# Optimization experiments

Measured on AMD Instinct MI355X. Metric: run time of the kernel, lower is better.

The kernel has to match this reference:

```python
import jax, jax.numpy as jnp
import numpy as np

N_LEVELS = 16
F_PER_LEVEL = 2
LOG2_T = 19
TABLE = 1 << LOG2_T
BASE_RES = 16.0
FINEST_RES = 512.0
PRIMES = jnp.array([1, 2654435761, 805459861, 3674653429, 2097192037, 1434869437], dtype=jnp.uint32)
# Hashing offsets: BOX_OFFSETS_6D enumerates dim0 in the OUTERMOST loop -> dim d uses bit (5-d) of vertex index.
OFF_HASH = jnp.array(((np.arange(64)[:, None] >> (5 - np.arange(6))) & 1).astype(np.int32))
# Interpolation weights use LSB-first bits (vertex_binary = [i >> d & 1]) -- faithful to the source (incl. its bit-order mismatch).
OFF_W = jnp.array(((np.arange(64)[:, None] >> np.arange(6)) & 1).astype(np.bool_))


def _hash6(coords):
    # coords: [..., 6] int32 -> int32 indices in [0, 2^19). uint32 wraparound matches torch int32 overflow + bitmask.
    u = coords.astype(jnp.uint32) * PRIMES
    h = u[..., 0]
    for d in range(1, 6):
        h = h ^ u[..., d]
    return (h & jnp.uint32(TABLE - 1)).astype(jnp.int32)


def _encode_level(emb, res, x):
    # emb: [T, F], res: scalar resolution, x: [B, 6] clamped to [0,1] box
    grid = 1.0 / res
    bl = jnp.floor(x * res).astype(jnp.int32)            # bottom-left voxel index, [B, 6]
    vmin = bl.astype(x.dtype) * grid                     # voxel_min_vertex
    w = jnp.clip((x - vmin) / (grid + 1e-6), 0.0, 1.0)   # [B, 6]
    verts = bl[:, None, :] + OFF_HASH[None]              # [B, 64, 6]
    ve = emb[_hash6(verts)]                              # gather: [B, 64, F]
    wv = jnp.where(OFF_W[None], w[:, None, :], 1.0 - w[:, None, :]).prod(-1)  # [B, 64]
    return jnp.einsum('bv,bvf->bf', wv, ve)


def hash_encode(x, embeddings):
    b = np.exp((np.log(FINEST_RES) - np.log(BASE_RES)) / (N_LEVELS - 1))
    res = jnp.maximum(jnp.floor(BASE_RES * b ** jnp.arange(N_LEVELS, dtype=jnp.float32)), 1.0)
    xc = jnp.clip(x, 0.0, 1.0)

    def body(carry, lv):
        emb, r = lv
        return carry, _encode_level(emb, r, xc)

    _, feats = jax.lax.scan(body, 0, (embeddings, res))  # [L, B, F]
    return jnp.transpose(feats, (1, 0, 2)).reshape(x.shape[0], N_LEVELS * F_PER_LEVEL)


def _mlp(W0, b0, Wres, bres, scales, Wout, bout, h):
    # NeRF_MLP_Residual_Scaled: initial -> (num_layers-1) scaled residual blocks -> output
    h = jax.nn.relu(h @ W0 + b0)
    for i in range(Wres.shape[0]):
        h = scales[i] * jax.nn.relu(h @ Wres[i] + bres[i]) + h
    return h @ Wout + bout


def setup_inputs() -> dict:
    key = jax.random.key(0)
    ks = jax.random.split(key, 10)
    B, C, H, IN, OUT = 524288, 4, 256, 32, 1
    NB = 3  # num_layers - 1 residual blocks
    x = jax.random.uniform(ks[0], (B, 6), jnp.float32)
    layer_id = jax.random.randint(ks[1], (B,), 0, C)
    embeddings = jax.random.uniform(ks[2], (N_LEVELS, TABLE, F_PER_LEVEL), jnp.float32, -1e-4, 1e-4)
    W0 = jax.random.normal(ks[3], (C, IN, H), jnp.float32) / np.sqrt(IN)
    b0 = jax.random.normal(ks[4], (C, H), jnp.float32) * 0.01
    Wres = jax.random.normal(ks[5], (C, NB, H, H), jnp.float32) / np.sqrt(H)
    bres = jax.random.normal(ks[6], (C, NB, H), jnp.float32) * 0.01
    scales = jax.random.normal(ks[7], (C, NB), jnp.float32) * 0.1
    Wout = jax.random.normal(ks[8], (C, H, OUT), jnp.float32) / np.sqrt(H)
    bout = jax.random.normal(ks[9], (C, OUT), jnp.float32) * 0.01
    return dict(x_6d_input=x, layer_id=layer_id, embeddings=embeddings, W0=W0, b0=b0,
                Wres=Wres, bres=bres, scales=scales, Wout=Wout, bout=bout)


def reference(x_6d_input, layer_id, embeddings, W0, b0, Wres, bres, scales, Wout, bout):
    enc = hash_encode(x_6d_input, embeddings)  # [B, 32]
    outs = jax.vmap(_mlp, in_axes=(0, 0, 0, 0, 0, 0, 0, None))(W0, b0, Wres, bres, scales, Wout, bout, enc)  # [C, B, out]
    midx = (layer_id % outs.shape[0]).astype(jnp.int32)
    return jnp.take_along_axis(outs, midx[None, :, None], axis=0)[0]  # [B, out]
```

## Files before the change

### kernel.cpp

```cpp
#include <hip/hip_runtime.h>
#include <stdint.h>

#define HTABLE (1u << 19)
#define TMASK  (HTABLE - 1u)
#define TILE   64
#define KSTR   264
#define KE     40

typedef __attribute__((ext_vector_type(8))) short short8;
typedef __attribute__((ext_vector_type(4))) float floatx4;

__device__ __forceinline__ float relu_(float v) { return fmaxf(v, 0.f); }

__device__ __forceinline__ uint32_t f2bf(float f) {
    uint32_t u = __float_as_uint(f);
    return (u + 0x7FFFu + ((u >> 16) & 1u)) >> 16;
}
__device__ __forceinline__ float bf2f(uint32_t h) { return __uint_as_float(h << 16); }

__device__ __forceinline__ uint32_t sel4(const uint4& v, uint32_t i) {
    uint32_t lo = (i & 1u) ? v.y : v.x;
    uint32_t hi = (i & 1u) ? v.w : v.z;
    return (i & 2u) ? hi : lo;
}

__device__ __constant__ uint32_t PRS[6] = {1u, 2654435761u, 805459861u, 3674653429u, 2097192037u, 1434869437u};
__device__ __constant__ float RESF[16]  = {16.f,20.f,25.f,32.f,40.f,50.f,64.f,80.f,101.f,128.f,161.f,203.f,256.f,322.f,406.f,512.f};
__device__ __constant__ float GRIDF[16] = {1.f/16.f,1.f/20.f,1.f/25.f,1.f/32.f,1.f/40.f,1.f/50.f,1.f/64.f,1.f/80.f,
                                           1.f/101.f,1.f/128.f,1.f/161.f,1.f/203.f,1.f/256.f,1.f/322.f,1.f/406.f,1.f/512.f};

__global__ void k_count(const int* __restrict__ lid, int n, int* __restrict__ cnt) {
    __shared__ int h4[4];
    int i = blockIdx.x * blockDim.x + threadIdx.x;
    if (threadIdx.x < 4) h4[threadIdx.x] = 0;
    __syncthreads();
    if (i < n) atomicAdd(&h4[lid[i] & 3], 1);
    __syncthreads();
    if (threadIdx.x < 4) atomicAdd(&cnt[threadIdx.x], h4[threadIdx.x]);
}

__global__ void k_offsets(const int* __restrict__ cnt, int* __restrict__ cursor) {
    if (threadIdx.x == 0 && blockIdx.x == 0) {
        int off = 0;
        for (int k = 0; k < 4; k++) {
            cursor[k] = off;
            off = (off + cnt[k] + 63) & ~63;
        }
    }
}

__global__ void k_scatter(const int* __restrict__ lid, int n, int* __restrict__ cursor, int* __restrict__ perm) {
    int i = blockIdx.x * blockDim.x + threadIdx.x;
    if (i >= n) return;
    int lane = threadIdx.x & 63;
    int c = lid[i] & 3;
    unsigned long long m0 = __ballot(c == 0), m1 = __ballot(c == 1);
    unsigned long long m2 = __ballot(c == 2), m3 = __ballot(c == 3);
    unsigned long long mc = (c == 0) ? m0 : (c == 1) ? m1 : (c == 2) ? m2 : m3;
    int rank = __popcll(mc & ((1ull << lane) - 1ull));
    int cntl = (lane == 0) ? __popcll(m0) : (lane == 1) ? __popcll(m1) : (lane == 2) ? __popcll(m2) : __popcll(m3);
    int basev = 0;
    if (lane < 4) basev = atomicAdd(&cursor[lane], cntl);
    int base = __shfl(basev, c, 64);
    perm[base + rank] = i;
}

__global__ __launch_bounds__(256) void k_packtab(const float* __restrict__ emb, uint32_t* __restrict__ T) {
    const int i = blockIdx.x * 256 + threadIdx.x;
    float2 e = ((const float2*)emb)[i];
    T[i] = f2bf(e.x) | (f2bf(e.y) << 16);
}

__global__ __launch_bounds__(256) void k_prep(const float* __restrict__ Wres, const float* __restrict__ W0,
                                              uint16_t* __restrict__ Wrt, uint16_t* __restrict__ W0t) {
    __shared__ float sm[64 * 65 > 32 * 257 ? 64 * 65 : 32 * 257];
    const int t = threadIdx.x;
    const int bid = blockIdx.x;
    if (bid < 192) {
        const int c = bid / 48, rem = bid % 48, ib = rem / 16, tile = rem % 16;
        const int n0 = (tile / 4) * 64, k0 = (tile % 4) * 64;
        const float* src = Wres + (size_t)(c * 3 + ib) * 65536;
        for (int i = 0; i < 16; i++) {
            int idx = t + 256 * i, r = idx >> 6, cc = idx & 63;
            sm[r * 65 + cc] = src[(size_t)(k0 + r) * 256 + n0 + cc];
        }
        __syncthreads();
        uint16_t* dst = Wrt + (size_t)(c * 3 + ib) * 65536;
        for (int i = 0; i < 16; i++) {
            int idx = t + 256 * i, rn = idx >> 6, ck = idx & 63;
            dst[(size_t)(n0 + rn) * 256 + k0 + ck] = (uint16_t)f2bf(sm[ck * 65 + rn]);
        }
    } else {
        const int c = bid - 192;
        for (int i = 0; i < 32; i++) {
            int idx = t + 256 * i, k = idx >> 8, n = idx & 255;
            sm[k * 257 + n] = W0[(size_t)c * 8192 + idx];
        }
        __syncthreads();
        for (int i = 0; i < 32; i++) {
            int idx = t + 256 * i, n = idx >> 5, k = idx & 31;
            W0t[(size_t)c * 8192 + idx] = (uint16_t)f2bf(sm[k * 257 + n]);
        }
    }
}

__global__ __launch_bounds__(256, 4) void k_encode(
    const float* __restrict__ x, const uint32_t* __restrict__ T,
    uint32_t* __restrict__ encP, int B)
{
    __shared__ float xs[256 * 6];
    const int t = threadIdx.x;
    const int NC8 = (B >> 8) << 3;
    const int pass = (blockIdx.x >= NC8) ? 1 : 0;
    const int rem  = blockIdx.x - pass * NC8;
    const int l    = (rem & 7) + (pass << 3);
    const int chunk = rem >> 3;
    const int pbase = chunk << 8;

    for (int idx = t; idx < 256 * 6; idx += 256) {
        float v = x[(size_t)pbase * 6 + idx];
        xs[idx] = fminf(fmaxf(v, 0.f), 1.f);
    }
    __syncthreads();

    const float res  = RESF[l];
    const float grid = GRIDF[l];
    float wv[6]; uint32_t ua[6], ub[6];
    #pragma unroll
    for (int d = 0; d < 6; d++) {
        float xv  = xs[t * 6 + d];
        float blf = floorf(xv * res);
        float w   = (xv - blf * grid) / (grid + 1e-6f);
        wv[d] = fminf(fmaxf(w, 0.f), 1.f);
        uint32_t uu = (uint32_t)(int)blf * PRS[d];
        ua[d] = uu; ub[d] = uu + PRS[d];
    }
    uint32_t HK[4]; float WK[4];
    #pragma unroll
    for (int q = 0; q < 4; q++) {
        const int b1 = (q >> 1) & 1, bb = q & 1;
        HK[q] = (b1 ? ub[4] : ua[4]) ^ (bb ? ub[5] : ua[5]);
        WK[q] = (bb ? wv[0] : 1.f - wv[0]) * (b1 ? wv[1] : 1.f - wv[1]);
    }
    uint32_t S8[8]; float W8[8];
    #pragma unroll
    for (int jj = 0; jj < 8; jj++) {
        const int j1 = jj >> 2, j = jj & 3;
        const int b1 = (j >> 1) & 1, bb = j & 1;
        const uint32_t hj = (b1 ? ub[2] : ua[2]) ^ (bb ? ub[3] : ua[3]);
        const float  wj = ((bb ? wv[2] : 1.f - wv[2]) * (b1 ? wv[3] : 1.f - wv[3]));
        S8[jj] = (j1 ? ub[1] : ua[1]) ^ hj;
        W8[jj] = (j1 ? wv[4] : 1.f - wv[4]) * wj;
    }
    const float w5a = 1.f - wv[5], w5b = wv[5];
    const uint32_t bl0  = ua[0];
    const uint32_t mask = bl0 ^ (bl0 + 1u);
    const uint32_t* __restrict__ Tl  = T + (size_t)l * HTABLE;
    const uint4*    __restrict__ Tl4 = reinterpret_cast<const uint4*>(Tl);

    float f0 = 0.f, f1 = 0.f;
    #pragma unroll 2
    for (int jj = 0; jj < 8; jj++) {
        const uint32_t Sj = S8[jj];
        const float   wj = W8[jj];
        #pragma unroll
        for (int k = 0; k < 4; k++) {
            const uint32_t h  = (bl0 ^ Sj ^ HK[k]) & TMASK;
            const float wS = wj * WK[k];
            uint32_t pa, pb;
            if (mask == 1u) {
                const uint2 pr = *(const uint2*)(Tl + (h & ~1u));
                pa = (h & 1u) ? pr.y : pr.x;
                pb = (h & 1u) ? pr.x : pr.y;
            } else if (mask == 3u) {
                const uint4 La = Tl4[h >> 2];
                const uint32_t i0 = h & 3u;
                pa = sel4(La, i0);
                pb = sel4(La, i0 ^ 3u);
            } else {
                pa = Tl[h];
                pb = Tl[h ^ mask];
            }
            const float e0x = __uint_as_float(pa << 16),  e0y = __uint_as_float(pa & 0xFFFF0000u);
            const float e1x = __uint_as_float(pb << 16),  e1y = __uint_as_float(pb & 0xFFFF0000u);
            f0 = fmaf(wS, fmaf(w5a, e0x, w5b * e1x), f0);
            f1 = fmaf(wS, fmaf(w5a, e0y, w5b * e1y), f1);
        }
    }
    encP[(size_t)l * B + pbase + t] = f2bf(f0) | (f2bf(f1) << 16);
}

__global__ __launch_bounds__(256, 2) void k_mlp2(
    const int* __restrict__ lid, const uint32_t* __restrict__ encP,
    const uint16_t* __restrict__ W0t, const float* __restrict__ b0,
    const uint16_t* __restrict__ Wrt, const float* __restrict__ bres,
    const float* __restrict__ scales, const float* __restrict__ Wout, const float* __restrict__ bout,
    const int* __restrict__ perm, float* __restrict__ out, int B)
{
    __shared__ uint16_t hB[64 * KSTR];
    __shared__ uint16_t encB[64 * KE];
    __shared__ float    bs[256];
    __shared__ float    outP[256];
    __shared__ int      permL[TILE];

    const int t  = threadIdx.x;
    const int lane = t & 63;
    const int wv = t >> 6;
    const int mi = lane & 15;
    const int q  = lane >> 4;

    if (t < TILE) permL[t] = perm[(size_t)blockIdx.x * TILE + t];
    __syncthreads();
    const int g0 = permL[0];
    if (g0 < 0) return;
    const int c = lid[g0] & 3;

    bs[t] = b0[c * 256 + t];
    for (int idx = t; idx < 16 * 64; idx += 256) {
        const int l = idx >> 6, pp = idx & 63;
        const int gi = permL[pp];
        ((uint32_t*)encB)[pp * (KE / 2) + l] = (gi >= 0) ? encP[(size_t)l * B + gi] : 0u;
    }
    __syncthreads();

    floatx4 acc[4][4];
    floatx4 h_reg[4][4];

    {
        #pragma unroll
        for (int mt = 0; mt < 4; mt++)
            #pragma unroll
            for (int nt = 0; nt < 4; nt++) acc[mt][nt] = (floatx4){0.f, 0.f, 0.f, 0.f};
        const short8* Wp = (const short8*)(W0t + (size_t)c * 8192);
        short8 A[4], Bf[4];
        #pragma unroll
        for (int mt = 0; mt < 4; mt++) A[mt] = Wp[(wv * 64 + mt * 16 + mi) * 4 + q];
        #pragma unroll
        for (int nt = 0; nt < 4; nt++) Bf[nt] = *(const short8*)&encB[(nt * 16 + mi) * KE + q * 8];
        #pragma unroll
        for (int mt = 0; mt < 4; mt++)
            #pragma unroll
            for (int nt = 0; nt < 4; nt++)
                acc[mt][nt] = __builtin_amdgcn_mfma_f32_16x16x32_bf16(A[mt], Bf[nt], acc[mt][nt], 0, 0, 0);
        #pragma unroll
        for (int mt = 0; mt < 4; mt++) {
            const int nb = wv * 64 + mt * 16 + q * 4;
            #pragma unroll
            for (int nt = 0; nt < 4; nt++) {
                floatx4 u = acc[mt][nt], h;
                h[0] = relu_(u[0] + bs[nb + 0]); h[1] = relu_(u[1] + bs[nb + 1]);
                h[2] = relu_(u[2] + bs[nb + 2]); h[3] = relu_(u[3] + bs[nb + 3]);
                h_reg[mt][nt] = h;
                uint2 pk; pk.x = f2bf(h[0]) | (f2bf(h[1]) << 16); pk.y = f2bf(h[2]) | (f2bf(h[3]) << 16);
                *(uint2*)&hB[(nt * 16 + mi) * KSTR + nb] = pk;
            }
        }
    }
    __syncthreads();

    #pragma unroll 1
    for (int ib = 0; ib < 3; ib++) {
        bs[t] = bres[(size_t)((c * 3 + ib) << 8) + t];
        const float s = scales[c * 3 + ib];
        #pragma unroll
        for (int mt = 0; mt < 4; mt++)
            #pragma unroll
            for (int nt = 0; nt < 4; nt++) acc[mt][nt] = (floatx4){0.f, 0.f, 0.f, 0.f};

        const short8* Wp = (const short8*)(Wrt + (size_t)(c * 3 + ib) * 65536);
        short8 Acur[4], Anext[4], Bf[4];
        #pragma unroll
        for (int mt = 0; mt < 4; mt++) Acur[mt] = Wp[(wv * 64 + mt * 16 + mi) * 32 + q];
        #pragma unroll 1
        for (int ks = 0; ks < 8; ks++) {
            #pragma unroll
            for (int nt = 0; nt < 4; nt++)
                Bf[nt] = *(const short8*)&hB[(nt * 16 + mi) * KSTR + ks * 32 + q * 8];
            if (ks < 7) {
                #pragma unroll
                for (int mt = 0; mt < 4; mt++)
                    Anext[mt] = Wp[(wv * 64 + mt * 16 + mi) * 32 + (ks + 1) * 4 + q];
            }
            #pragma unroll
            for (int mt = 0; mt < 4; mt++)
                #pragma unroll
                for (int nt = 0; nt < 4; nt++)
                    acc[mt][nt] = __builtin_amdgcn_mfma_f32_16x16x32_bf16(Acur[mt], Bf[nt], acc[mt][nt], 0, 0, 0);
            #pragma unroll
            for (int mt = 0; mt < 4; mt++) Acur[mt] = Anext[mt];
        }
        __syncthreads();
        #pragma unroll
        for (int mt = 0; mt < 4; mt++) {
            const int nb = wv * 64 + mt * 16 + q * 4;
            #pragma unroll
            for (int nt = 0; nt < 4; nt++) {
                floatx4 u = acc[mt][nt];
                floatx4 h = h_reg[mt][nt];
                h[0] = fmaf(s, relu_(u[0] + bs[nb + 0]), h[0]);
                h[1] = fmaf(s, relu_(u[1] + bs[nb + 1]), h[1]);
                h[2] = fmaf(s, relu_(u[2] + bs[nb + 2]), h[2]);
                h[3] = fmaf(s, relu_(u[3] + bs[nb + 3]), h[3]);
                h_reg[mt][nt] = h;
                if (ib < 2) {
                    uint2 pk; pk.x = f2bf(h[0]) | (f2bf(h[1]) << 16); pk.y = f2bf(h[2]) | (f2bf(h[3]) << 16);
                    *(uint2*)&hB[(nt * 16 + mi) * KSTR + nb] = pk;
                }
            }
        }
        if (ib < 2) __syncthreads();
    }

    __syncthreads();
    bs[t] = Wout[c * 256 + t];
    __syncthreads();
    float po[4] = {0.f, 0.f, 0.f, 0.f};
    #pragma unroll
    for (int mt = 0; mt < 4; mt++) {
        const int nb = wv * 64 + mt * 16 + q * 4;
        const float w0v = bs[nb + 0], w1v = bs[nb + 1], w2v = bs[nb + 2], w3v = bs[nb + 3];
        #pragma unroll
        for (int nt = 0; nt < 4; nt++) {
            const floatx4 h = h_reg[mt][nt];
            po[nt] += h[0] * w0v + h[1] * w1v + h[2] * w2v + h[3] * w3v;
        }
    }
    #pragma unroll
    for (int nt = 0; nt < 4; nt++) {
        float v = po[nt];
        v += __shfl_xor(v, 16, 64);
        v += __shfl_xor(v, 32, 64);
        if (q == 0) outP[wv * 64 + nt * 16 + mi] = v;
    }
    __syncthreads();
    if (t < TILE) {
        float r = outP[t] + outP[64 + t] + outP[128 + t] + outP[192 + t] + bout[c];
        const int gi = permL[t];
        if (gi >= 0) out[gi] = r;
    }
}

extern "C" void kernel_launch(void* const* d_in, const int* in_sizes, int n_in,
                              void* d_out, int out_size, void* d_ws, size_t ws_size,
                              hipStream_t stream) {
    const float* x      = (const float*)d_in[0];
    const int*   lid    = (const int*)  d_in[1];
    const float* emb    = (const float*)d_in[2];
    const float* W0     = (const float*)d_in[3];
    const float* b0     = (const float*)d_in[4];
    const float* Wres   = (const float*)d_in[5];
    const float* bres   = (const float*)d_in[6];
    const float* scales = (const float*)d_in[7];
    const float* Wout   = (const float*)d_in[8];
    const float* bout   = (const float*)d_in[9];
    float* out = (float*)d_out;

    const int B = in_sizes[1];
    int* cnt    = (int*)d_ws;
    int* cursor = cnt + 4;
    int* perm   = cnt + 64;
    uint16_t* W0t = (uint16_t*)((char*)d_ws + 2228224);
    uint16_t* Wrt = (uint16_t*)((char*)d_ws + 2359296);
    uint32_t* encP = (uint32_t*)((char*)d_ws + (4u << 20));
    uint32_t* T    = (uint32_t*)((char*)d_ws + (36u << 20));
    const int nblk = B / TILE + 4;

    (void)hipMemsetAsync(d_ws, 0, 32, stream);
    (void)hipMemsetAsync(perm, 0xFF, (size_t)nblk * TILE * sizeof(int), stream);
    k_packtab<<<(16 * (int)HTABLE) / 256, 256, 0, stream>>>(emb, T);
    k_prep   <<<196, 256, 0, stream>>>(Wres, W0, Wrt, W0t);
    k_count  <<<B / 256, 256, 0, stream>>>(lid, B, cnt);
    k_offsets<<<1, 64, 0, stream>>>(cnt, cursor);
    k_scatter<<<B / 256, 256, 0, stream>>>(lid, B, cursor, perm);
    k_encode <<<(B / 256) * 16, 256, 0, stream>>>(x, T, encP, B);
    k_mlp2   <<<nblk, 256, 0, stream>>>(lid, encP, W0t, b0, Wrt, bres, scales, Wout, bout, perm, out, B);
}
```

Baseline: 1.767 ms.

## Fuse hash encoding and MLP into persistent work-queue kernel over sorted points

Replaces the separate encode and MLP kernels with one persistent kernel of 512 blocks. Blocks pull tasks from eight per-XCD atomic queues, and each queue interleaves encode chunks with MLP tiles that spin-wait on per-chunk completion counters. The scatter pass now also permutes x into class-sorted order, so encoding writes directly in tile order and the MLP reads contiguous encodings without an indirect gather. This is meant to overlap the gather-bound encoding with the MFMA-bound MLP and to avoid a kernel boundary. In exchange it adds spin-wait latency, atomics, hardcoded sizes (NCHUNK, NTILE) tied to the batch size, and a risk of deadlock if producer ordering is not guaranteed.

Measured after the change: 4.138 ms. 134% more time.

```diff
diff --git a/kernel.cpp b/kernel.cpp
--- a/kernel.cpp
+++ b/kernel.cpp
@@ -7,6 +7,12 @@
 #define KSTR   264
 #define KE     40
 
+#define NTILE   8196
+#define NCHUNK  2049
+#define BPAD    (NCHUNK * 256)
+#define MACROS  259
+#define NTQ     (MACROS * 20)
+
 typedef __attribute__((ext_vector_type(8))) short short8;
 typedef __attribute__((ext_vector_type(4))) float floatx4;
 
@@ -16,7 +22,6 @@
     uint32_t u = __float_as_uint(f);
     return (u + 0x7FFFu + ((u >> 16) & 1u)) >> 16;
 }
-__device__ __forceinline__ float bf2f(uint32_t h) { return __uint_as_float(h << 16); }
 
 __device__ __forceinline__ uint32_t sel4(const uint4& v, uint32_t i) {
     uint32_t lo = (i & 1u) ? v.y : v.x;
@@ -49,7 +54,8 @@
     }
 }
 
-__global__ void k_scatter(const int* __restrict__ lid, int n, int* __restrict__ cursor, int* __restrict__ perm) {
+__global__ void k_scatter(const int* __restrict__ lid, const float* __restrict__ x, int n,
+                          int* __restrict__ cursor, int* __restrict__ perm, float* __restrict__ xp) {
     int i = blockIdx.x * blockDim.x + threadIdx.x;
     if (i >= n) return;
     int lane = threadIdx.x & 63;
@@ -62,7 +68,12 @@
     int basev = 0;
     if (lane < 4) basev = atomicAdd(&cursor[lane], cntl);
     int base = __shfl(basev, c, 64);
-    perm[base + rank] = i;
+    int dst = base + rank;
+    perm[dst] = i;
+    const float2* xr = (const float2*)(x + (size_t)i * 6);
+    float2* xw = (float2*)(xp + (size_t)dst * 6);
+    float2 a = xr[0], b = xr[1], cc = xr[2];
+    xw[0] = a; xw[1] = b; xw[2] = cc;
 }
 
 __global__ __launch_bounds__(256) void k_packtab(const float* __restrict__ emb, uint32_t* __restrict__ T) {
@@ -104,239 +115,272 @@
     }
 }
 
-__global__ __launch_bounds__(256, 4) void k_encode(
-    const float* __restrict__ x, const uint32_t* __restrict__ T,
-    uint32_t* __restrict__ encP, int B)
-{
-    __shared__ float xs[256 * 6];
-    const int t = threadIdx.x;
-    const int NC8 = (B >> 8) << 3;
-    const int pass = (blockIdx.x >= NC8) ? 1 : 0;
-    const int rem  = blockIdx.x - pass * NC8;
-    const int l    = (rem & 7) + (pass << 3);
-    const int chunk = rem >> 3;
-    const int pbase = chunk << 8;
-
-    for (int idx = t; idx < 256 * 6; idx += 256) {
-        float v = x[(size_t)pbase * 6 + idx];
-        xs[idx] = fminf(fmaxf(v, 0.f), 1.f);
-    }
-    __syncthreads();
-
-    const float res  = RESF[l];
-    const float grid = GRIDF[l];
-    float wv[6]; uint32_t ua[6], ub[6];
-    #pragma unroll
-    for (int d = 0; d < 6; d++) {
-        float xv  = xs[t * 6 + d];
-        float blf = floorf(xv * res);
-        float w   = (xv - blf * grid) / (grid + 1e-6f);
-        wv[d] = fminf(fmaxf(w, 0.f), 1.f);
-        uint32_t uu = (uint32_t)(int)blf * PRS[d];
-        ua[d] = uu; ub[d] = uu + PRS[d];
-    }
-    uint32_t HK[4]; float WK[4];
-    #pragma unroll
-    for (int q = 0; q < 4; q++) {
-        const int b1 = (q >> 1) & 1, bb = q & 1;
-        HK[q] = (b1 ? ub[4] : ua[4]) ^ (bb ? ub[5] : ua[5]);
-        WK[q] = (bb ? wv[0] : 1.f - wv[0]) * (b1 ? wv[1] : 1.f - wv[1]);
-    }
-    uint32_t S8[8]; float W8[8];
-    #pragma unroll
-    for (int jj = 0; jj < 8; jj++) {
-        const int j1 = jj >> 2, j = jj & 3;
-        const int b1 = (j >> 1) & 1, bb = j & 1;
-        const uint32_t hj = (b1 ? ub[2] : ua[2]) ^ (bb ? ub[3] : ua[3]);
-        const float  wj = ((bb ? wv[2] : 1.f - wv[2]) * (b1 ? wv[3] : 1.f - wv[3]));
-        S8[jj] = (j1 ? ub[1] : ua[1]) ^ hj;
-        W8[jj] = (j1 ? wv[4] : 1.f - wv[4]) * wj;
-    }
-    const float w5a = 1.f - wv[5], w5b = wv[5];
-    const uint32_t bl0  = ua[0];
-    const uint32_t mask = bl0 ^ (bl0 + 1u);
-    const uint32_t* __restrict__ Tl  = T + (size_t)l * HTABLE;
-    const uint4*    __restrict__ Tl4 = reinterpret_cast<const uint4*>(Tl);
-
-    float f0 = 0.f, f1 = 0.f;
-    #pragma unroll 2
-    for (int jj = 0; jj < 8; jj++) {
-        const uint32_t Sj = S8[jj];
-        const float   wj = W8[jj];
-        #pragma unroll
-        for (int k = 0; k < 4; k++) {
-            const uint32_t h  = (bl0 ^ Sj ^ HK[k]) & TMASK;
-            const float wS = wj * WK[k];
-            uint32_t pa, pb;
-            if (mask == 1u) {
-                const uint2 pr = *(const uint2*)(Tl + (h & ~1u));
-                pa = (h & 1u) ? pr.y : pr.x;
-                pb = (h & 1u) ? pr.x : pr.y;
-            } else if (mask == 3u) {
-                const uint4 La = Tl4[h >> 2];
-                const uint32_t i0 = h & 3u;
-                pa = sel4(La, i0);
-                pb = sel4(La, i0 ^ 3u);
-            } else {
-                pa = Tl[h];
-                pb = Tl[h ^ mask];
-            }
-            const float e0x = __uint_as_float(pa << 16),  e0y = __uint_as_float(pa & 0xFFFF0000u);
-            const float e1x = __uint_as_float(pb << 16),  e1y = __uint_as_float(pb & 0xFFFF0000u);
-            f0 = fmaf(wS, fmaf(w5a, e0x, w5b * e1x), f0);
-            f1 = fmaf(wS, fmaf(w5a, e0y, w5b * e1y), f1);
-        }
-    }
-    encP[(size_t)l * B + pbase + t] = f2bf(f0) | (f2bf(f1) << 16);
-}
-
-__global__ __launch_bounds__(256, 2) void k_mlp2(
-    const int* __restrict__ lid, const uint32_t* __restrict__ encP,
+__global__ __launch_bounds__(256, 2) void k_fused(
+    const float* __restrict__ xp, const uint32_t* __restrict__ T,
+    uint32_t* __restrict__ encQ,
+    const int* __restrict__ lid, const int* __restrict__ perm,
     const uint16_t* __restrict__ W0t, const float* __restrict__ b0,
     const uint16_t* __restrict__ Wrt, const float* __restrict__ bres,
     const float* __restrict__ scales, const float* __restrict__ Wout, const float* __restrict__ bout,
-    const int* __restrict__ perm, float* __restrict__ out, int B)
+    float* __restrict__ out,
+    unsigned int* __restrict__ qt, unsigned int* __restrict__ done)
 {
-    __shared__ uint16_t hB[64 * KSTR];
-    __shared__ uint16_t encB[64 * KE];
-    __shared__ float    bs[256];
-    __shared__ float    outP[256];
-    __shared__ int      permL[TILE];
-
-    const int t  = threadIdx.x;
-    const int lane = t & 63;
-    const int wv = t >> 6;
-    const int mi = lane & 15;
-    const int q  = lane >> 4;
-
-    if (t < TILE) permL[t] = perm[(size_t)blockIdx.x * TILE + t];
-    __syncthreads();
-    const int g0 = permL[0];
-    if (g0 < 0) return;
-    const int c = lid[g0] & 3;
-
-    bs[t] = b0[c * 256 + t];
-    for (int idx = t; idx < 16 * 64; idx += 256) {
-        const int l = idx >> 6, pp = idx & 63;
-        const int gi = permL[pp];
-        ((uint32_t*)encB)[pp * (KE / 2) + l] = (gi >= 0) ? encP[(size_t)l * B + gi] : 0u;
-    }
-    __syncthreads();
-
-    floatx4 acc[4][4];
-    floatx4 h_reg[4][4];
-
-    {
-        #pragma unroll
-        for (int mt = 0; mt < 4; mt++)
-            #pragma unroll
-            for (int nt = 0; nt < 4; nt++) acc[mt][nt] = (floatx4){0.f, 0.f, 0.f, 0.f};
-        const short8* Wp = (const short8*)(W0t + (size_t)c * 8192);
-        short8 A[4], Bf[4];
-        #pragma unroll
-        for (int mt = 0; mt < 4; mt++) A[mt] = Wp[(wv * 64 + mt * 16 + mi) * 4 + q];
-        #pragma unroll
-        for (int nt = 0; nt < 4; nt++) Bf[nt] = *(const short8*)&encB[(nt * 16 + mi) * KE + q * 8];
-        #pragma unroll
-        for (int mt = 0; mt < 4; mt++)
-            #pragma unroll
-            for (int nt = 0; nt < 4; nt++)
-                acc[mt][nt] = __builtin_amdgcn_mfma_f32_16x16x32_bf16(A[mt], Bf[nt], acc[mt][nt], 0, 0, 0);
-        #pragma unroll
-        for (int mt = 0; mt < 4; mt++) {
-            const int nb = wv * 64 + mt * 16 + q * 4;
-            #pragma unroll
-            for (int nt = 0; nt < 4; nt++) {
-                floatx4 u = acc[mt][nt], h;
-                h[0] = relu_(u[0] + bs[nb + 0]); h[1] = relu_(u[1] + bs[nb + 1]);
-                h[2] = relu_(u[2] + bs[nb + 2]); h[3] = relu_(u[3] + bs[nb + 3]);
-                h_reg[mt][nt] = h;
-                uint2 pk; pk.x = f2bf(h[0]) | (f2bf(h[1]) << 16); pk.y = f2bf(h[2]) | (f2bf(h[3]) << 16);
-                *(uint2*)&hB[(nt * 16 + mi) * KSTR + nb] = pk;
+    __shared__ __align__(16) char smem[41216];
+    __shared__ int sh_q, sh_r;
+    const int t = threadIdx.x;
+    const int xcd0 = blockIdx.x & 7;
+
+    for (;;) {
+        if (t == 0) {
+            int q = -1; int r = 0;
+            for (int a = 0; a < 8; a++) {
+                int qq = (xcd0 + a) & 7;
+                unsigned rr = __hip_atomic_fetch_add(&qt[qq], 1u, __ATOMIC_RELAXED, __HIP_MEMORY_SCOPE_AGENT);
+                if (rr < (unsigned)NTQ) { q = qq; r = (int)rr; break; }
             }
-        }
-    }
-    __syncthreads();
-
-    #pragma unroll 1
-    for (int ib = 0; ib < 3; ib++) {
-        bs[t] = bres[(size_t)((c * 3 + ib) << 8) + t];
-        const float s = scales[c * 3 + ib];
-        #pragma unroll
-        for (int mt = 0; mt < 4; mt++)
-            #pragma unroll
-            for (int nt = 0; nt < 4; nt++) acc[mt][nt] = (floatx4){0.f, 0.f, 0.f, 0.f};
-
-        const short8* Wp = (const short8*)(Wrt + (size_t)(c * 3 + ib) * 65536);
-        short8 Acur[4], Anext[4], Bf[4];
-        #pragma unroll
-        for (int mt = 0; mt < 4; mt++) Acur[mt] = Wp[(wv * 64 + mt * 16 + mi) * 32 + q];
-        #pragma unroll 1
-        for (int ks = 0; ks < 8; ks++) {
-            #pragma unroll
-            for (int nt = 0; nt < 4; nt++)
-                Bf[nt] = *(const short8*)&hB[(nt * 16 + mi) * KSTR + ks * 32 + q * 8];
-            if (ks < 7) {
+            sh_q = q; sh_r = r;
+        }
+        __syncthreads();
+        const int q = sh_q, r = sh_r;
+        if (q < 0) break;
+        const int m = r / 20, s = r - m * 20;
+
+        if (s < 16) {
+            const int chunk = m * 8 + (s >> 1);
+            if (chunk < NCHUNK) {
+                const int l = q + 8 * (s & 1);
+                float* xs = (float*)smem;
+                const int pbase = chunk << 8;
+                for (int idx = t; idx < 256 * 6; idx += 256) {
+                    float v = xp[(size_t)pbase * 6 + idx];
+                    xs[idx] = fminf(fmaxf(v, 0.f), 1.f);
+                }
+                __syncthreads();
+
+                const float res  = RESF[l];
+                const float grid = GRIDF[l];
+                float wv[6]; uint32_t ua[6], ub[6];
                 #pragma unroll
-                for (int mt = 0; mt < 4; mt++)
-                    Anext[mt] = Wp[(wv * 64 + mt * 16 + mi) * 32 + (ks + 1) * 4 + q];
+                for (int d = 0; d < 6; d++) {
+                    float xv  = xs[t * 6 + d];
+                    float blf = floorf(xv * res);
+                    float w   = (xv - blf * grid) / (grid + 1e-6f);
+                    wv[d] = fminf(fmaxf(w, 0.f), 1.f);
+                    uint32_t uu = (uint32_t)(int)blf * PRS[d];
+                    ua[d] = uu; ub[d] = uu + PRS[d];
+                }
+                uint32_t HK[4]; float WK[4];
+                #pragma unroll
+                for (int qq = 0; qq < 4; qq++) {
+                    const int b1 = (qq >> 1) & 1, bb = qq & 1;
+                    HK[qq] = (b1 ? ub[4] : ua[4]) ^ (bb ? ub[5] : ua[5]);
+                    WK[qq] = (bb ? wv[0] : 1.f - wv[0]) * (b1 ? wv[1] : 1.f - wv[1]);
+                }
+                uint32_t S8[8]; float W8[8];
+                #pragma unroll
+                for (int jj = 0; jj < 8; jj++) {
+                    const int j1 = jj >> 2, j = jj & 3;
+                    const int b1 = (j >> 1) & 1, bb = j & 1;
+                    const uint32_t hj = (b1 ? ub[2] : ua[2]) ^ (bb ? ub[3] : ua[3]);
+                    const float  wj = ((bb ? wv[2] : 1.f - wv[2]) * (b1 ? wv[3] : 1.f - wv[3]));
+                    S8[jj] = (j1 ? ub[1] : ua[1]) ^ hj;
+                    W8[jj] = (j1 ? wv[4] : 1.f - wv[4]) * wj;
+                }
+                const float w5a = 1.f - wv[5], w5b = wv[5];
+                const uint32_t bl0  = ua[0];
+                const uint32_t mask = bl0 ^ (bl0 + 1u);
+                const uint32_t* __restrict__ Tl  = T + (size_t)l * HTABLE;
+                const uint4*    __restrict__ Tl4 = reinterpret_cast<const uint4*>(Tl);
+
+                float f0 = 0.f, f1 = 0.f;
+                #pragma unroll 4
+                for (int jj = 0; jj < 8; jj++) {
+                    const uint32_t Sj = S8[jj];
+                    const float   wj = W8[jj];
+                    #pragma unroll
+                    for (int k = 0; k < 4; k++) {
+                        const uint32_t h  = (bl0 ^ Sj ^ HK[k]) & TMASK;
+                        const float wS = wj * WK[k];
+                        uint32_t pa, pb;
+                        if (mask == 1u) {
+                            const uint2 pr = *(const uint2*)(Tl + (h & ~1u));
+                            pa = (h & 1u) ? pr.y : pr.x;
+                            pb = (h & 1u) ? pr.x : pr.y;
+                        } else if (mask == 3u) {
+                            const uint4 La = Tl4[h >> 2];
+                            const uint32_t i0 = h & 3u;
+                            pa = sel4(La, i0);
+                            pb = sel4(La, i0 ^ 3u);
+                        } else {
+                            pa = Tl[h];
+                            pb = Tl[h ^ mask];
+                        }
+                        const float e0x = __uint_as_float(pa << 16),  e0y = __uint_as_float(pa & 0xFFFF0000u);
+                        const float e1x = __uint_as_float(pb << 16),  e1y = __uint_as_float(pb & 0xFFFF0000u);
+                        f0 = fmaf(wS, fmaf(w5a, e0x, w5b * e1x), f0);
+                        f1 = fmaf(wS, fmaf(w5a, e0y, w5b * e1y), f1);
+                    }
+                }
+                const uint32_t val = f2bf(f0) | (f2bf(f1) << 16);
+                __hip_atomic_store(&encQ[(size_t)l * BPAD + pbase + t], val,
+                                   __ATOMIC_RELAXED, __HIP_MEMORY_SCOPE_AGENT);
+                asm volatile("s_waitcnt vmcnt(0)" ::: "memory");
+                __syncthreads();
+                if (t == 0)
+                    __hip_atomic_fetch_add(&done[chunk], 1u, __ATOMIC_RELAXED, __HIP_MEMORY_SCOPE_AGENT);
             }
-            #pragma unroll
-            for (int mt = 0; mt < 4; mt++)
-                #pragma unroll
-                for (int nt = 0; nt < 4; nt++)
-                    acc[mt][nt] = __builtin_amdgcn_mfma_f32_16x16x32_bf16(Acur[mt], Bf[nt], acc[mt][nt], 0, 0, 0);
-            #pragma unroll
-            for (int mt = 0; mt < 4; mt++) Acur[mt] = Anext[mt];
+        } else {
+            const int grp = 8 * (m - 2) + q;
+            if (m >= 2 && grp < NCHUNK) {
+                const int tile = 4 * grp + (s - 16);
+                uint16_t* hB   = (uint16_t*)smem;
+                uint16_t* encB = (uint16_t*)(smem + 33792);
+                float*    bs   = (float*)(smem + 38912);
+                float*    outP = (float*)(smem + 39936);
+                int*      permL= (int*)(smem + 40960);
+
+                const int lane = t & 63;
+                const int wv = t >> 6;
+                const int mi = lane & 15;
+                const int qd = lane >> 4;
+
+                if (t < TILE) permL[t] = perm[(size_t)tile * TILE + t];
+                if (t == 0) {
+                    while (__hip_atomic_load(&done[grp], __ATOMIC_RELAXED, __HIP_MEMORY_SCOPE_AGENT) < 16u)
+                        __builtin_amdgcn_s_sleep(8);
+                }
+                __syncthreads();
+                const int g0 = permL[0];
+                if (g0 >= 0) {
+                    const int c = lid[g0] & 3;
+                    bs[t] = b0[c * 256 + t];
+                    for (int idx = t; idx < 16 * 64; idx += 256) {
+                        const int l = idx >> 6, pp = idx & 63;
+                        ((uint32_t*)encB)[pp * (KE / 2) + l] =
+                            __hip_atomic_load(&encQ[(size_t)l * BPAD + (size_t)tile * 64 + pp],
+                                              __ATOMIC_RELAXED, __HIP_MEMORY_SCOPE_AGENT);
+                    }
+                    __syncthreads();
+
+                    floatx4 acc[4][4];
+                    floatx4 h_reg[4][4];
+
+                    {
+                        #pragma unroll
+                        for (int mt = 0; mt < 4; mt++)
+                            #pragma unroll
+                            for (int nt = 0; nt < 4; nt++) acc[mt][nt] = (floatx4){0.f, 0.f, 0.f, 0.f};
+                        const short8* Wp = (const short8*)(W0t + (size_t)c * 8192);
+                        short8 A[4], Bf[4];
+                        #pragma unroll
+                        for (int mt = 0; mt < 4; mt++) A[mt] = Wp[(wv * 64 + mt * 16 + mi) * 4 + qd];
+                        #pragma unroll
+                        for (int nt = 0; nt < 4; nt++) Bf[nt] = *(const short8*)&encB[(nt * 16 + mi) * KE + qd * 8];
+                        #pragma unroll
+                        for (int mt = 0; mt < 4; mt++)
+                            #pragma unroll
+                            for (int nt = 0; nt < 4; nt++)
+                                acc[mt][nt] = __builtin_amdgcn_mfma_f32_16x16x32_bf16(A[mt], Bf[nt], acc[mt][nt], 0, 0, 0);
+                        #pragma unroll
+                        for (int mt = 0; mt < 4; mt++) {
+                            const int nb = wv * 64 + mt * 16 + qd * 4;
+                            #pragma unroll
+                            for (int nt = 0; nt < 4; nt++) {
+                                floatx4 u = acc[mt][nt], h;
+                                h[0] = relu_(u[0] + bs[nb + 0]); h[1] = relu_(u[1] + bs[nb + 1]);
+                                h[2] = relu_(u[2] + bs[nb + 2]); h[3] = relu_(u[3] + bs[nb + 3]);
+                                h_reg[mt][nt] = h;
+                                uint2 pk; pk.x = f2bf(h[0]) | (f2bf(h[1]) << 16); pk.y = f2bf(h[2]) | (f2bf(h[3]) << 16);
+                                *(uint2*)&hB[(nt * 16 + mi) * KSTR + nb] = pk;
+                            }
+                        }
+                    }
+                    __syncthreads();
+
+                    #pragma unroll 1
+                    for (int ib = 0; ib < 3; ib++) {
+                        bs[t] = bres[(size_t)((c * 3 + ib) << 8) + t];
+                        const float sc = scales[c * 3 + ib];
+                        #pragma unroll
+                        for (int mt = 0; mt < 4; mt++)
+                            #pragma unroll
+                            for (int nt = 0; nt < 4; nt++) acc[mt][nt] = (floatx4){0.f, 0.f, 0.f, 0.f};
+
+                        const short8* Wp = (const short8*)(Wrt + (size_t)(c * 3 + ib) * 65536);
+                        short8 Acur[4], Anext[4], Bf[4];
+                        #pragma unroll
+                        for (int mt = 0; mt < 4; mt++) Acur[mt] = Wp[(wv * 64 + mt * 16 + mi) * 32 + qd];
+                        #pragma unroll 1
+                        for (int ks = 0; ks < 8; ks++) {
+                            #pragma unroll
+                            for (int nt = 0; nt < 4; nt++)
+                                Bf[nt] = *(const short8*)&hB[(nt * 16 + mi) * KSTR + ks * 32 + qd * 8];
+                            if (ks < 7) {
+                                #pragma unroll
+                                for (int mt = 0; mt < 4; mt++)
+                                    Anext[mt] = Wp[(wv * 64 + mt * 16 + mi) * 32 + (ks + 1) * 4 + qd];
+                            }
+                            #pragma unroll
+                            for (int mt = 0; mt < 4; mt++)
+                                #pragma unroll
+                                for (int nt = 0; nt < 4; nt++)
+                                    acc[mt][nt] = __builtin_amdgcn_mfma_f32_16x16x32_bf16(Acur[mt], Bf[nt], acc[mt][nt], 0, 0, 0);
+                            #pragma unroll
+                            for (int mt = 0; mt < 4; mt++) Acur[mt] = Anext[mt];
+                        }
+                        __syncthreads();
+                        #pragma unroll
+                        for (int mt = 0; mt < 4; mt++) {
+                            const int nb = wv * 64 + mt * 16 + qd * 4;
+                            #pragma unroll
+                            for (int nt = 0; nt < 4; nt++) {
+                                floatx4 u = acc[mt][nt];
+                                floatx4 h = h_reg[mt][nt];
+                                h[0] = fmaf(sc, relu_(u[0] + bs[nb + 0]), h[0]);
+                                h[1] = fmaf(sc, relu_(u[1] + bs[nb + 1]), h[1]);
+                                h[2] = fmaf(sc, relu_(u[2] + bs[nb + 2]), h[2]);
+                                h[3] = fmaf(sc, relu_(u[3] + bs[nb + 3]), h[3]);
+                                h_reg[mt][nt] = h;
+                                if (ib < 2) {
+                                    uint2 pk; pk.x = f2bf(h[0]) | (f2bf(h[1]) << 16); pk.y = f2bf(h[2]) | (f2bf(h[3]) << 16);
+                                    *(uint2*)&hB[(nt * 16 + mi) * KSTR + nb] = pk;
+                                }
+                            }
+                        }
+                        if (ib < 2) __syncthreads();
+                    }
+
+                    __syncthreads();
+                    bs[t] = Wout[c * 256 + t];
+                    __syncthreads();
+                    float po[4] = {0.f, 0.f, 0.f, 0.f};
+                    #pragma unroll
+                    for (int mt = 0; mt < 4; mt++) {
+                        const int nb = wv * 64 + mt * 16 + qd * 4;
+                        const float w0v = bs[nb + 0], w1v = bs[nb + 1], w2v = bs[nb + 2], w3v = bs[nb + 3];
+                        #pragma unroll
+                        for (int nt = 0; nt < 4; nt++) {
+                            const floatx4 h = h_reg[mt][nt];
+                            po[nt] += h[0] * w0v + h[1] * w1v + h[2] * w2v + h[3] * w3v;
+                        }
+                    }
+                    #pragma unroll
+                    for (int nt = 0; nt < 4; nt++) {
+                        float v = po[nt];
+                        v += __shfl_xor(v, 16, 64);
+                        v += __shfl_xor(v, 32, 64);
+                        if (qd == 0) outP[wv * 64 + nt * 16 + mi] = v;
+                    }
+                    __syncthreads();
+                    if (t < TILE) {
+                        float rr = outP[t] + outP[64 + t] + outP[128 + t] + outP[192 + t] + bout[c];
+                        const int gi = permL[t];
+                        if (gi >= 0) out[gi] = rr;
+                    }
+                }
+            }
         }
         __syncthreads();
-        #pragma unroll
-        for (int mt = 0; mt < 4; mt++) {
-            const int nb = wv * 64 + mt * 16 + q * 4;
-            #pragma unroll
-            for (int nt = 0; nt < 4; nt++) {
-                floatx4 u = acc[mt][nt];
-                floatx4 h = h_reg[mt][nt];
-                h[0] = fmaf(s, relu_(u[0] + bs[nb + 0]), h[0]);
-                h[1] = fmaf(s, relu_(u[1] + bs[nb + 1]), h[1]);
-                h[2] = fmaf(s, relu_(u[2] + bs[nb + 2]), h[2]);
-                h[3] = fmaf(s, relu_(u[3] + bs[nb + 3]), h[3]);
-                h_reg[mt][nt] = h;
-                if (ib < 2) {
-                    uint2 pk; pk.x = f2bf(h[0]) | (f2bf(h[1]) << 16); pk.y = f2bf(h[2]) | (f2bf(h[3]) << 16);
-                    *(uint2*)&hB[(nt * 16 + mi) * KSTR + nb] = pk;
-                }
-            }
-        }
-        if (ib < 2) __syncthreads();
-    }
-
-    __syncthreads();
-    bs[t] = Wout[c * 256 + t];
-    __syncthreads();
-    float po[4] = {0.f, 0.f, 0.f, 0.f};
-    #pragma unroll
-    for (int mt = 0; mt < 4; mt++) {
-        const int nb = wv * 64 + mt * 16 + q * 4;
-        const float w0v = bs[nb + 0], w1v = bs[nb + 1], w2v = bs[nb + 2], w3v = bs[nb + 3];
-        #pragma unroll
-        for (int nt = 0; nt < 4; nt++) {
-            const floatx4 h = h_reg[mt][nt];
-            po[nt] += h[0] * w0v + h[1] * w1v + h[2] * w2v + h[3] * w3v;
-        }
-    }
-    #pragma unroll
-    for (int nt = 0; nt < 4; nt++) {
-        float v = po[nt];
-        v += __shfl_xor(v, 16, 64);
-        v += __shfl_xor(v, 32, 64);
-        if (q == 0) outP[wv * 64 + nt * 16 + mi] = v;
-    }
-    __syncthreads();
-    if (t < TILE) {
-        float r = outP[t] + outP[64 + t] + outP[128 + t] + outP[192 + t] + bout[c];
-        const int gi = permL[t];
-        if (gi >= 0) out[gi] = r;
     }
 }
 
@@ -358,20 +402,22 @@
     const int B = in_sizes[1];
     int* cnt    = (int*)d_ws;
     int* cursor = cnt + 4;
-    int* perm   = cnt + 64;
-    uint16_t* W0t = (uint16_t*)((char*)d_ws + 2228224);
-    uint16_t* Wrt = (uint16_t*)((char*)d_ws + 2359296);
-    uint32_t* encP = (uint32_t*)((char*)d_ws + (4u << 20));
-    uint32_t* T    = (uint32_t*)((char*)d_ws + (36u << 20));
-    const int nblk = B / TILE + 4;
-
-    (void)hipMemsetAsync(d_ws, 0, 32, stream);
-    (void)hipMemsetAsync(perm, 0xFF, (size_t)nblk * TILE * sizeof(int), stream);
+    unsigned int* qt   = (unsigned int*)((char*)d_ws + 64);
+    unsigned int* done = (unsigned int*)((char*)d_ws + 256);
+    int*      perm = (int*)((char*)d_ws + 16384);
+    uint16_t* W0t  = (uint16_t*)((char*)d_ws + 2228224);
+    uint16_t* Wrt  = (uint16_t*)((char*)d_ws + 2359296);
+    uint32_t* encQ = (uint32_t*)((char*)d_ws + (4ull  << 20));
+    uint32_t* T    = (uint32_t*)((char*)d_ws + (38ull << 20));
+    float*    xp   = (float*)   ((char*)d_ws + (70ull << 20));
+
+    (void)hipMemsetAsync(d_ws, 0, 16384, stream);
+    (void)hipMemsetAsync(perm, 0xFF, (size_t)NTILE * TILE * sizeof(int), stream);
     k_packtab<<<(16 * (int)HTABLE) / 256, 256, 0, stream>>>(emb, T);
     k_prep   <<<196, 256, 0, stream>>>(Wres, W0, Wrt, W0t);
     k_count  <<<B / 256, 256, 0, stream>>>(lid, B, cnt);
     k_offsets<<<1, 64, 0, stream>>>(cnt, cursor);
-    k_scatter<<<B / 256, 256, 0, stream>>>(lid, B, cursor, perm);
-    k_encode <<<(B / 256) * 16, 256, 0, stream>>>(x, T, encP, B);
-    k_mlp2   <<<nblk, 256, 0, stream>>>(lid, encP, W0t, b0, Wrt, bres, scales, Wout, bout, perm, out, B);
-}
+    k_scatter<<<B / 256, 256, 0, stream>>>(lid, x, B, cursor, perm, xp);
+    k_fused  <<<512, 256, 0, stream>>>(xp, T, encQ, lid, perm, W0t, b0, Wrt, bres,
+                                       scales, Wout, bout, out, qt, done);
+}
```
